# Performance work log

Hardware: AMD Instinct MI355X
Metric: run time of the kernel (lower is better)

## Reference

```python
import jax, jax.numpy as jnp
import numpy as np

NUM_NODES = 1_000_000
MEM_DIM = 128
MSG_DIM = 128
B = 262_144


def setup_inputs() -> dict:
    key = jax.random.key(0)
    k1, k2, k3, k4, k5, k6, k7 = jax.random.split(key, 7)
    s = 1.0 / np.sqrt(MEM_DIM)
    return {
        "memory": jax.random.normal(k1, (NUM_NODES, MEM_DIM), jnp.float32) * 0.1,
        "last_update": jnp.zeros((NUM_NODES,), jnp.float32),
        "messages": jax.random.normal(k2, (B, MSG_DIM), jnp.float32),
        "timestamps": jax.random.uniform(k3, (B,), jnp.float32),
        "W_ih": jax.random.uniform(k4, (3 * MEM_DIM, MSG_DIM), jnp.float32, -s, s),
        "W_hh": jax.random.uniform(k5, (3 * MEM_DIM, MEM_DIM), jnp.float32, -s, s),
        "b_ih": jax.random.uniform(k6, (3 * MEM_DIM,), jnp.float32, -s, s),
        "b_hh": jax.random.uniform(k7, (3 * MEM_DIM,), jnp.float32, -s, s),
        "node_ids": jax.random.randint(jax.random.fold_in(key, 99), (B,), 0, NUM_NODES, jnp.int64 if jax.config.jax_enable_x64 else jnp.int32),
    }


def gru_cell(x, h, W_ih, W_hh, b_ih, b_hh):
    # torch.nn.GRUCell math
    gi = x @ W_ih.T + b_ih  # [B, 3H]
    gh = h @ W_hh.T + b_hh  # [B, 3H]
    i_r, i_z, i_n = jnp.split(gi, 3, axis=-1)
    h_r, h_z, h_n = jnp.split(gh, 3, axis=-1)
    r = jax.nn.sigmoid(i_r + h_r)
    z = jax.nn.sigmoid(i_z + h_z)
    n = jnp.tanh(i_n + r * h_n)
    return (1.0 - z) * n + z * h


def reference(memory, last_update, messages, timestamps, W_ih, W_hh, b_ih, b_hh, node_ids):
    # gather node memory rows
    h = memory[node_ids]  # [B, MEM_DIM]
    h_new = gru_cell(messages, h, W_ih, W_hh, b_ih, b_hh)
    # scatter updated state and timestamps back into persistent buffers
    memory_new = memory.at[node_ids].set(h_new)
    last_update_new = last_update.at[node_ids].set(timestamps)
    return memory_new, last_update_new
```

## Files before the change

### kernel.cpp

```cpp
#include <hip/hip_runtime.h>
#include <hip/hip_bf16.h>
#include <stdint.h>

#define NN   1000000
#define DD   128
#define BT   262144
#define TR   64
#define RPB  512
#define NT   (RPB / TR)
#define GRUB (BT / RPB)
#define WINBIT (1 << 30)

typedef __attribute__((ext_vector_type(8))) short bf16x8;
typedef __attribute__((ext_vector_type(4))) float f32x4;

__device__ __forceinline__ uint32_t f2bf2(float lo, float hi) {
    __hip_bfloat162 b = __float22bfloat162_rn(make_float2(lo, hi));
    uint32_t u; __builtin_memcpy(&u, &b, 4); return u;
}
__device__ __forceinline__ bf16x8 cvt8(float4 a, float4 b) {
    union { bf16x8 v; uint32_t u[4]; } r;
    r.u[0] = f2bf2(a.x, a.y);
    r.u[1] = f2bf2(a.z, a.w);
    r.u[2] = f2bf2(b.x, b.y);
    r.u[3] = f2bf2(b.z, b.w);
    return r.v;
}
__device__ __forceinline__ float bf2f(unsigned short s) {
    union { uint32_t u; float f; } c; c.u = ((uint32_t)s) << 16;
    return c.f;
}
__device__ __forceinline__ float fastrcp(float x) {
    return __builtin_amdgcn_rcpf(x);
}
__device__ __forceinline__ float sigmoid_f(float x) {
    return fastrcp(1.0f + __expf(-x));
}
__device__ __forceinline__ float tanh_f(float x) {
    return fmaf(2.0f, fastrcp(1.0f + __expf(-2.0f * x)), -1.0f);
}

__global__ __launch_bounds__(256) void k_init(int4* __restrict__ winner) {
    int i = blockIdx.x * 256 + threadIdx.x;
    if (i < NN / 4) winner[i] = make_int4(-1, -1, -1, -1);
}

__global__ __launch_bounds__(256) void k_winner(const int* __restrict__ node_ids,
                                                int* __restrict__ winner) {
    int i = blockIdx.x * 256 + threadIdx.x;
    if (i < BT) atomicMax(&winner[node_ids[i]], i);
}

__global__ __launch_bounds__(256) void k_copy(const float4* __restrict__ mem_in,
                                              const float* __restrict__ lu_in,
                                              const float* __restrict__ ts,
                                              const int* __restrict__ winner,
                                              float4* __restrict__ mem_out,
                                              float* __restrict__ lu_out) {
    const long NV4 = (long)NN * 32;
    const long TOTAL = NV4 + NN;
    long stride = (long)gridDim.x * 256;
    for (long i = blockIdx.x * 256L + threadIdx.x; i < TOTAL; i += stride) {
        if (i < NV4) {
            int node = (int)(i >> 5);
            if (winner[node] < 0) mem_out[i] = mem_in[i];
        } else {
            int v = (int)(i - NV4);
            int w = winner[v];
            lu_out[v] = (w >= 0) ? ts[w] : lu_in[v];
        }
    }
}

__global__ __launch_bounds__(512, 2) void k_gru(const float* __restrict__ memory,
                                                const float* __restrict__ messages,
                                                const float* __restrict__ W_ih,
                                                const float* __restrict__ W_hh,
                                                const float* __restrict__ b_ih,
                                                const float* __restrict__ b_hh,
                                                const int* __restrict__ node_ids,
                                                const int* __restrict__ winner,
                                                float* __restrict__ out_mem) {
    __shared__ unsigned short x_lds[2][TR * DD];
    __shared__ unsigned short h_lds[2][TR * DD];
    __shared__ int s_nid[RPB];

    const int tid = threadIdx.x;
    const int rowBase = blockIdx.x * RPB;

    for (int i = tid; i < RPB; i += 512) {
        int brow = rowBase + i;
        int nid = node_ids[brow];
        s_nid[i] = nid | ((winner[nid] == brow) ? WINBIT : 0);
    }
    __syncthreads();

    const int lane  = tid & 63;
    const int wave  = tid >> 6;
    const int l15   = lane & 15;
    const int khalf = lane >> 4;
    const int jcol  = wave * 16 + l15;

    bf16x8 wf[6][4];
#pragma unroll
    for (int g = 0; g < 3; ++g) {
#pragma unroll
        for (int ks = 0; ks < 4; ++ks) {
            const float* p = W_ih + (size_t)(g * 128 + jcol) * DD + ks * 32 + khalf * 8;
            wf[g][ks] = cvt8(*(const float4*)p, *(const float4*)(p + 4));
            const float* q = W_hh + (size_t)(g * 128 + jcol) * DD + ks * 32 + khalf * 8;
            wf[3 + g][ks] = cvt8(*(const float4*)q, *(const float4*)(q + 4));
        }
    }
    const float br = b_ih[jcol] + b_hh[jcol];
    const float bz = b_ih[128 + jcol] + b_hh[128 + jcol];
    const float bin = b_ih[256 + jcol];
    const float bhn = b_hh[256 + jcol];

    const int sr  = tid >> 4;
    const int sc8 = (tid & 15) * 8;
    const int swz = (sc8 * 2) ^ ((sr & 7) << 4);
    const int offH0 = sr * 256 + swz;
    const int offH1 = (32 + sr) * 256 + swz;

#define GLOAD(X0, X1, H0, H1, t, half)                                          \
    {                                                                           \
        int r_ = (t) * TR + (half) * 32 + sr;                                   \
        const float* xp_ = messages + (size_t)(rowBase + r_) * DD + sc8;        \
        X0 = ((const float4*)xp_)[0]; X1 = ((const float4*)xp_)[1];             \
        const float* hp_ = memory + (size_t)(s_nid[r_] & (WINBIT - 1)) * DD + sc8; \
        H0 = ((const float4*)hp_)[0]; H1 = ((const float4*)hp_)[1];             \
    }

    float4 xA0, xA1, hA0, hA1, xB0, xB1, hB0, hB1;
    GLOAD(xA0, xA1, hA0, hA1, 0, 0);
    GLOAD(xB0, xB1, hB0, hB1, 0, 1);

#pragma unroll 1
    for (int t = 0; t < NT; ++t) {
        const int buf = t & 1;
        char* xb = (char*)(&x_lds[buf][0]);
        char* hb = (char*)(&h_lds[buf][0]);
        *(bf16x8*)(xb + offH0) = cvt8(xA0, xA1);
        *(bf16x8*)(hb + offH0) = cvt8(hA0, hA1);
        *(bf16x8*)(xb + offH1) = cvt8(xB0, xB1);
        *(bf16x8*)(hb + offH1) = cvt8(hB0, hB1);
        if (t + 1 < NT) {
            GLOAD(xA0, xA1, hA0, hA1, t + 1, 0);
            GLOAD(xB0, xB1, hB0, hB1, t + 1, 1);
        }
        asm volatile("s_waitcnt lgkmcnt(0)" ::: "memory");
        __builtin_amdgcn_sched_barrier(0);
        __builtin_amdgcn_s_barrier();
        __builtin_amdgcn_sched_barrier(0);

#pragma unroll
        for (int sub = 0; sub < 4; ++sub) {
            const int arow = sub * 16 + l15;
            const char* xr = (const char*)(&x_lds[buf][0]) + arow * 256;
            const char* hr = (const char*)(&h_lds[buf][0]) + arow * 256;
            const int aswz = (arow & 7) << 4;
            bf16x8 ax[4], ah[4];
#pragma unroll
            for (int ks = 0; ks < 4; ++ks) {
                const int cb = (ks * 64 + khalf * 16) ^ aswz;
                ax[ks] = *(const bf16x8*)(xr + cb);
                ah[ks] = *(const bf16x8*)(hr + cb);
            }
            f32x4 a_r  = {br,  br,  br,  br};
            f32x4 a_z  = {bz,  bz,  bz,  bz};
            f32x4 a_in = {bin, bin, bin, bin};
            f32x4 a_hn = {bhn, bhn, bhn, bhn};
#pragma unroll
            for (int ks = 0; ks < 4; ++ks) {
                a_r  = __builtin_amdgcn_mfma_f32_16x16x32_bf16(ax[ks], wf[0][ks], a_r,  0, 0, 0);
                a_r  = __builtin_amdgcn_mfma_f32_16x16x32_bf16(ah[ks], wf[3][ks], a_r,  0, 0, 0);
                a_z  = __builtin_amdgcn_mfma_f32_16x16x32_bf16(ax[ks], wf[1][ks], a_z,  0, 0, 0);
                a_z  = __builtin_amdgcn_mfma_f32_16x16x32_bf16(ah[ks], wf[4][ks], a_z,  0, 0, 0);
                a_in = __builtin_amdgcn_mfma_f32_16x16x32_bf16(ax[ks], wf[2][ks], a_in, 0, 0, 0);
                a_hn = __builtin_amdgcn_mfma_f32_16x16x32_bf16(ah[ks], wf[5][ks], a_hn, 0, 0, 0);
            }
#pragma unroll
            for (int q = 0; q < 4; ++q) {
                const int rl = sub * 16 + khalf * 4 + q;
                const int tr = t * TR + rl;
                float rg = sigmoid_f(a_r[q]);
                float zg = sigmoid_f(a_z[q]);
                float ng = tanh_f(a_in[q] + rg * a_hn[q]);
                unsigned short hu = *(const unsigned short*)(
                    (const char*)(&h_lds[buf][0]) + rl * 256 + ((jcol * 2) ^ ((rl & 7) << 4)));
                float h = bf2f(hu);
                float hnew = fmaf(zg, h - ng, ng);
                int v = s_nid[tr];
                if (v & WINBIT)
                    out_mem[(size_t)(v & (WINBIT - 1)) * DD + jcol] = hnew;
            }
        }
    }
#undef GLOAD
}

extern "C" void kernel_launch(void* const* d_in, const int* in_sizes, int n_in,
                              void* d_out, int out_size, void* d_ws, size_t ws_size,
                              hipStream_t stream) {
    const float* memory      = (const float*)d_in[0];
    const float* last_update = (const float*)d_in[1];
    const float* messages    = (const float*)d_in[2];
    const float* timestamps  = (const float*)d_in[3];
    const float* W_ih        = (const float*)d_in[4];
    const float* W_hh        = (const float*)d_in[5];
    const float* b_ih        = (const float*)d_in[6];
    const float* b_hh        = (const float*)d_in[7];
    const int*   node_ids    = (const int*)d_in[8];

    float* out_mem = (float*)d_out;
    float* out_lu  = out_mem + (size_t)NN * DD;

    int* winner = (int*)d_ws;

    k_init<<<(NN / 4 + 255) / 256, 256, 0, stream>>>((int4*)winner);
    k_winner<<<BT / 256, 256, 0, stream>>>(node_ids, winner);
    k_copy<<<4096, 256, 0, stream>>>((const float4*)memory, last_update, timestamps,
                                     winner, (float4*)out_mem, out_lu);
    k_gru<<<GRUB, 512, 0, stream>>>(memory, messages, W_ih, W_hh, b_ih, b_hh,
                                    node_ids, winner, out_mem);
}
```

Baseline: 282.9 us.

## Stage GRU inputs via direct global-to-LDS loads with fp32 tiles

Measured after the change: 493.0 us. 74.3% more time.

```diff
diff --git a/kernel.cpp b/kernel.cpp
--- a/kernel.cpp
+++ b/kernel.cpp
@@ -5,7 +5,7 @@
 #define NN   1000000
 #define DD   128
 #define BT   262144
-#define TR   64
+#define TR   32
 #define RPB  512
 #define NT   (RPB / TR)
 #define GRUB (BT / RPB)
@@ -26,9 +26,13 @@
     r.u[3] = f2bf2(b.z, b.w);
     return r.v;
 }
-__device__ __forceinline__ float bf2f(unsigned short s) {
-    union { uint32_t u; float f; } c; c.u = ((uint32_t)s) << 16;
-    return c.f;
+__device__ __forceinline__ bf16x8 cvt8v(f32x4 a, f32x4 b) {
+    union { bf16x8 v; uint32_t u[4]; } r;
+    r.u[0] = f2bf2(a[0], a[1]);
+    r.u[1] = f2bf2(a[2], a[3]);
+    r.u[2] = f2bf2(b[0], b[1]);
+    r.u[3] = f2bf2(b[2], b[3]);
+    return r.v;
 }
 __device__ __forceinline__ float fastrcp(float x) {
     return __builtin_amdgcn_rcpf(x);
@@ -38,6 +42,11 @@
 }
 __device__ __forceinline__ float tanh_f(float x) {
     return fmaf(2.0f, fastrcp(1.0f + __expf(-2.0f * x)), -1.0f);
+}
+__device__ __forceinline__ void glds16(const float* g, void* l) {
+    __builtin_amdgcn_global_load_lds(
+        (const __attribute__((address_space(1))) uint32_t*)g,
+        (__attribute__((address_space(3))) uint32_t*)l, 16, 0, 0);
 }
 
 __global__ __launch_bounds__(256) void k_init(int4* __restrict__ winner) {
@@ -72,7 +81,7 @@
     }
 }
 
-__global__ __launch_bounds__(512, 2) void k_gru(const float* __restrict__ memory,
+__global__ __launch_bounds__(512, 4) void k_gru(const float* __restrict__ memory,
                                                 const float* __restrict__ messages,
                                                 const float* __restrict__ W_ih,
                                                 const float* __restrict__ W_hh,
@@ -81,8 +90,8 @@
                                                 const int* __restrict__ node_ids,
                                                 const int* __restrict__ winner,
                                                 float* __restrict__ out_mem) {
-    __shared__ unsigned short x_lds[2][TR * DD];
-    __shared__ unsigned short h_lds[2][TR * DD];
+    __shared__ float x_lds[2][TR * DD];
+    __shared__ float h_lds[2][TR * DD];
     __shared__ int s_nid[RPB];
 
     const int tid = threadIdx.x;
@@ -112,73 +121,66 @@
             wf[3 + g][ks] = cvt8(*(const float4*)q, *(const float4*)(q + 4));
         }
     }
-    const float br = b_ih[jcol] + b_hh[jcol];
-    const float bz = b_ih[128 + jcol] + b_hh[128 + jcol];
+    const float br  = b_ih[jcol] + b_hh[jcol];
+    const float bz  = b_ih[128 + jcol] + b_hh[128 + jcol];
     const float bin = b_ih[256 + jcol];
     const float bhn = b_hh[256 + jcol];
 
-    const int sr  = tid >> 4;
-    const int sc8 = (tid & 15) * 8;
-    const int swz = (sc8 * 2) ^ ((sr & 7) << 4);
-    const int offH0 = sr * 256 + swz;
-    const int offH1 = (32 + sr) * 256 + swz;
-
-#define GLOAD(X0, X1, H0, H1, t, half)                                          \
-    {                                                                           \
-        int r_ = (t) * TR + (half) * 32 + sr;                                   \
-        const float* xp_ = messages + (size_t)(rowBase + r_) * DD + sc8;        \
-        X0 = ((const float4*)xp_)[0]; X1 = ((const float4*)xp_)[1];             \
-        const float* hp_ = memory + (size_t)(s_nid[r_] & (WINBIT - 1)) * DD + sc8; \
-        H0 = ((const float4*)hp_)[0]; H1 = ((const float4*)hp_)[1];             \
-    }
-
-    float4 xA0, xA1, hA0, hA1, xB0, xB1, hB0, hB1;
-    GLOAD(xA0, xA1, hA0, hA1, 0, 0);
-    GLOAD(xB0, xB1, hB0, hB1, 0, 1);
+    const int lrow0 = tid >> 5;
+    const int scc   = (tid & 31) ^ (lrow0 & 7);
+    const int ldsw0 = wave * 1024;
+    const int ldsw1 = wave * 1024 + 8192;
+
+#define STAGE(t, b)                                                              \
+    {                                                                            \
+        const int r0_ = (t) * TR + lrow0;                                        \
+        const float* xs0_ = messages + (size_t)(rowBase + r0_) * DD + scc * 4;   \
+        const float* xs1_ = messages + (size_t)(rowBase + r0_ + 16) * DD + scc * 4; \
+        const float* hs0_ = memory + (size_t)(s_nid[r0_] & (WINBIT - 1)) * DD + scc * 4; \
+        const float* hs1_ = memory + (size_t)(s_nid[r0_ + 16] & (WINBIT - 1)) * DD + scc * 4; \
+        glds16(xs0_, (char*)(&x_lds[b][0]) + ldsw0);                             \
+        glds16(xs1_, (char*)(&x_lds[b][0]) + ldsw1);                             \
+        glds16(hs0_, (char*)(&h_lds[b][0]) + ldsw0);                             \
+        glds16(hs1_, (char*)(&h_lds[b][0]) + ldsw1);                             \
+    }
+
+    STAGE(0, 0);
+    STAGE(1, 1);
 
 #pragma unroll 1
     for (int t = 0; t < NT; ++t) {
         const int buf = t & 1;
-        char* xb = (char*)(&x_lds[buf][0]);
-        char* hb = (char*)(&h_lds[buf][0]);
-        *(bf16x8*)(xb + offH0) = cvt8(xA0, xA1);
-        *(bf16x8*)(hb + offH0) = cvt8(hA0, hA1);
-        *(bf16x8*)(xb + offH1) = cvt8(xB0, xB1);
-        *(bf16x8*)(hb + offH1) = cvt8(hB0, hB1);
-        if (t + 1 < NT) {
-            GLOAD(xA0, xA1, hA0, hA1, t + 1, 0);
-            GLOAD(xB0, xB1, hB0, hB1, t + 1, 1);
-        }
-        asm volatile("s_waitcnt lgkmcnt(0)" ::: "memory");
+        if (t + 1 < NT) { asm volatile("s_waitcnt vmcnt(4)" ::: "memory"); }
+        else            { asm volatile("s_waitcnt vmcnt(0)" ::: "memory"); }
         __builtin_amdgcn_sched_barrier(0);
         __builtin_amdgcn_s_barrier();
         __builtin_amdgcn_sched_barrier(0);
 
 #pragma unroll
-        for (int sub = 0; sub < 4; ++sub) {
+        for (int sub = 0; sub < 2; ++sub) {
             const int arow = sub * 16 + l15;
-            const char* xr = (const char*)(&x_lds[buf][0]) + arow * 256;
-            const char* hr = (const char*)(&h_lds[buf][0]) + arow * 256;
-            const int aswz = (arow & 7) << 4;
-            bf16x8 ax[4], ah[4];
-#pragma unroll
-            for (int ks = 0; ks < 4; ++ks) {
-                const int cb = (ks * 64 + khalf * 16) ^ aswz;
-                ax[ks] = *(const bf16x8*)(xr + cb);
-                ah[ks] = *(const bf16x8*)(hr + cb);
-            }
+            const char* xb = (const char*)(&x_lds[buf][0]) + arow * 512;
+            const char* hb = (const char*)(&h_lds[buf][0]) + arow * 512;
+            const int as = arow & 7;
             f32x4 a_r  = {br,  br,  br,  br};
             f32x4 a_z  = {bz,  bz,  bz,  bz};
             f32x4 a_in = {bin, bin, bin, bin};
             f32x4 a_hn = {bhn, bhn, bhn, bhn};
 #pragma unroll
             for (int ks = 0; ks < 4; ++ks) {
-                a_r  = __builtin_amdgcn_mfma_f32_16x16x32_bf16(ax[ks], wf[0][ks], a_r,  0, 0, 0);
-                a_r  = __builtin_amdgcn_mfma_f32_16x16x32_bf16(ah[ks], wf[3][ks], a_r,  0, 0, 0);
-                a_z  = __builtin_amdgcn_mfma_f32_16x16x32_bf16(ax[ks], wf[1][ks], a_z,  0, 0, 0);
-                a_z  = __builtin_amdgcn_mfma_f32_16x16x32_bf16(ah[ks], wf[4][ks], a_z,  0, 0, 0);
-                a_in = __builtin_amdgcn_mfma_f32_16x16x32_bf16(ax[ks], wf[2][ks], a_in, 0, 0, 0);
-                a_hn = __builtin_amdgcn_mfma_f32_16x16x32_bf16(ah[ks], wf[5][ks], a_hn, 0, 0, 0);
+                const int c0 = ks * 8 + khalf * 2;
+                f32x4 x0 = *(const f32x4*)(xb + ((c0 ^ as) * 16));
+                f32x4 x1 = *(const f32x4*)(xb + (((c0 + 1) ^ as) * 16));
+                f32x4 h0 = *(const f32x4*)(hb + ((c0 ^ as) * 16));
+                f32x4 h1 = *(const f32x4*)(hb + (((c0 + 1) ^ as) * 16));
+                bf16x8 axk = cvt8v(x0, x1);
+                bf16x8 ahk = cvt8v(h0, h1);
+                a_r  = __builtin_amdgcn_mfma_f32_16x16x32_bf16(axk, wf[0][ks], a_r,  0, 0, 0);
+                a_r  = __builtin_amdgcn_mfma_f32_16x16x32_bf16(ahk, wf[3][ks], a_r,  0, 0, 0);
+                a_z  = __builtin_amdgcn_mfma_f32_16x16x32_bf16(axk, wf[1][ks], a_z,  0, 0, 0);
+                a_z  = __builtin_amdgcn_mfma_f32_16x16x32_bf16(ahk, wf[4][ks], a_z,  0, 0, 0);
+                a_in = __builtin_amdgcn_mfma_f32_16x16x32_bf16(axk, wf[2][ks], a_in, 0, 0, 0);
+                a_hn = __builtin_amdgcn_mfma_f32_16x16x32_bf16(ahk, wf[5][ks], a_hn, 0, 0, 0);
             }
 #pragma unroll
             for (int q = 0; q < 4; ++q) {
@@ -187,17 +189,20 @@
                 float rg = sigmoid_f(a_r[q]);
                 float zg = sigmoid_f(a_z[q]);
                 float ng = tanh_f(a_in[q] + rg * a_hn[q]);
-                unsigned short hu = *(const unsigned short*)(
-                    (const char*)(&h_lds[buf][0]) + rl * 256 + ((jcol * 2) ^ ((rl & 7) << 4)));
-                float h = bf2f(hu);
+                float h = h_lds[buf][rl * 128 + (((jcol >> 2) ^ (rl & 7)) * 4) + (jcol & 3)];
                 float hnew = fmaf(zg, h - ng, ng);
                 int v = s_nid[tr];
                 if (v & WINBIT)
                     out_mem[(size_t)(v & (WINBIT - 1)) * DD + jcol] = hnew;
             }
         }
-    }
-#undef GLOAD
+
+        __builtin_amdgcn_sched_barrier(0);
+        __builtin_amdgcn_s_barrier();
+        __builtin_amdgcn_sched_barrier(0);
+        if (t + 2 < NT) STAGE(t + 2, buf);
+    }
+#undef STAGE
 }
 
 extern "C" void kernel_launch(void* const* d_in, const int* in_sizes, int n_in,
```

## Fuse bulk memory copy and last_update scatter into GRU kernel

Applied to the files above, without the earlier changes.

After: 462.2 us. 63.4% more time.

```diff
diff --git a/kernel.cpp b/kernel.cpp
--- a/kernel.cpp
+++ b/kernel.cpp
@@ -10,6 +10,7 @@
 #define NT   (RPB / TR)
 #define GRUB (BT / RPB)
 #define WINBIT (1 << 30)
+#define NV4  32000000L
 
 typedef __attribute__((ext_vector_type(8))) short bf16x8;
 typedef __attribute__((ext_vector_type(4))) float f32x4;
@@ -49,27 +50,6 @@
                                                 int* __restrict__ winner) {
     int i = blockIdx.x * 256 + threadIdx.x;
     if (i < BT) atomicMax(&winner[node_ids[i]], i);
-}
-
-__global__ __launch_bounds__(256) void k_copy(const float4* __restrict__ mem_in,
-                                              const float* __restrict__ lu_in,
-                                              const float* __restrict__ ts,
-                                              const int* __restrict__ winner,
-                                              float4* __restrict__ mem_out,
-                                              float* __restrict__ lu_out) {
-    const long NV4 = (long)NN * 32;
-    const long TOTAL = NV4 + NN;
-    long stride = (long)gridDim.x * 256;
-    for (long i = blockIdx.x * 256L + threadIdx.x; i < TOTAL; i += stride) {
-        if (i < NV4) {
-            int node = (int)(i >> 5);
-            if (winner[node] < 0) mem_out[i] = mem_in[i];
-        } else {
-            int v = (int)(i - NV4);
-            int w = winner[v];
-            lu_out[v] = (w >= 0) ? ts[w] : lu_in[v];
-        }
-    }
 }
 
 __global__ __launch_bounds__(512, 2) void k_gru(const float* __restrict__ memory,
@@ -80,7 +60,10 @@
                                                 const float* __restrict__ b_hh,
                                                 const int* __restrict__ node_ids,
                                                 const int* __restrict__ winner,
-                                                float* __restrict__ out_mem) {
+                                                const float* __restrict__ lu_in,
+                                                const float* __restrict__ ts,
+                                                float* __restrict__ out_mem,
+                                                float* __restrict__ out_lu) {
     __shared__ unsigned short x_lds[2][TR * DD];
     __shared__ unsigned short h_lds[2][TR * DD];
     __shared__ int s_nid[RPB];
@@ -112,8 +95,8 @@
             wf[3 + g][ks] = cvt8(*(const float4*)q, *(const float4*)(q + 4));
         }
     }
-    const float br = b_ih[jcol] + b_hh[jcol];
-    const float bz = b_ih[128 + jcol] + b_hh[128 + jcol];
+    const float br  = b_ih[jcol] + b_hh[jcol];
+    const float bz  = b_ih[128 + jcol] + b_hh[128 + jcol];
     const float bin = b_ih[256 + jcol];
     const float bhn = b_hh[256 + jcol];
 
@@ -122,6 +105,9 @@
     const int swz = (sc8 * 2) ^ ((sr & 7) << 4);
     const int offH0 = sr * 256 + swz;
     const int offH1 = (32 + sr) * 256 + swz;
+
+    const float4* mem4 = (const float4*)memory;
+    float4* out4 = (float4*)out_mem;
 
 #define GLOAD(X0, X1, H0, H1, t, half)                                          \
     {                                                                           \
@@ -196,8 +182,22 @@
                     out_mem[(size_t)(v & (WINBIT - 1)) * DD + jcol] = hnew;
             }
         }
+
+        {
+            const long base4 = ((long)(blockIdx.x * NT + t)) * 8192 + tid;
+#pragma unroll
+            for (int k = 0; k < 16; ++k) {
+                long f = base4 + (long)k * 512;
+                if (f < NV4 && winner[(int)(f >> 5)] < 0) out4[f] = mem4[f];
+            }
+        }
     }
 #undef GLOAD
+
+    for (int i = blockIdx.x * 512 + tid; i < NN; i += GRUB * 512) {
+        int w = winner[i];
+        out_lu[i] = (w >= 0) ? ts[w] : lu_in[i];
+    }
 }
 
 extern "C" void kernel_launch(void* const* d_in, const int* in_sizes, int n_in,
@@ -220,8 +220,7 @@
 
     k_init<<<(NN / 4 + 255) / 256, 256, 0, stream>>>((int4*)winner);
     k_winner<<<BT / 256, 256, 0, stream>>>(node_ids, winner);
-    k_copy<<<4096, 256, 0, stream>>>((const float4*)memory, last_update, timestamps,
-                                     winner, (float4*)out_mem, out_lu);
     k_gru<<<GRUB, 512, 0, stream>>>(memory, messages, W_ih, W_hh, b_ih, b_hh,
-                                    node_ids, winner, out_mem);
-}
+                                    node_ids, winner, last_update, timestamps,
+                                    out_mem, out_lu);
+}
```

## Reorder gather prefetch in GRU loop, ping-pong h registers, raise occupancy bound

Applied to the files above, without the earlier changes.

Measured after the change: 508.6 us. +79.8%, slower.

```diff
diff --git a/kernel.cpp b/kernel.cpp
--- a/kernel.cpp
+++ b/kernel.cpp
@@ -72,7 +72,7 @@
     }
 }
 
-__global__ __launch_bounds__(512, 2) void k_gru(const float* __restrict__ memory,
+__global__ __launch_bounds__(512, 4) void k_gru(const float* __restrict__ memory,
                                                 const float* __restrict__ messages,
                                                 const float* __restrict__ W_ih,
                                                 const float* __restrict__ W_hh,
@@ -112,8 +112,8 @@
             wf[3 + g][ks] = cvt8(*(const float4*)q, *(const float4*)(q + 4));
         }
     }
-    const float br = b_ih[jcol] + b_hh[jcol];
-    const float bz = b_ih[128 + jcol] + b_hh[128 + jcol];
+    const float br  = b_ih[jcol] + b_hh[jcol];
+    const float bz  = b_ih[128 + jcol] + b_hh[128 + jcol];
     const float bin = b_ih[256 + jcol];
     const float bhn = b_hh[256 + jcol];
 
@@ -123,81 +123,101 @@
     const int offH0 = sr * 256 + swz;
     const int offH1 = (32 + sr) * 256 + swz;
 
-#define GLOAD(X0, X1, H0, H1, t, half)                                          \
+#define GLOADX(t)                                                               \
     {                                                                           \
-        int r_ = (t) * TR + (half) * 32 + sr;                                   \
-        const float* xp_ = messages + (size_t)(rowBase + r_) * DD + sc8;        \
-        X0 = ((const float4*)xp_)[0]; X1 = ((const float4*)xp_)[1];             \
-        const float* hp_ = memory + (size_t)(s_nid[r_] & (WINBIT - 1)) * DD + sc8; \
-        H0 = ((const float4*)hp_)[0]; H1 = ((const float4*)hp_)[1];             \
-    }
-
-    float4 xA0, xA1, hA0, hA1, xB0, xB1, hB0, hB1;
-    GLOAD(xA0, xA1, hA0, hA1, 0, 0);
-    GLOAD(xB0, xB1, hB0, hB1, 0, 1);
+        int r_ = (t) * TR + sr;                                                 \
+        const float* xp0_ = messages + (size_t)(rowBase + r_) * DD + sc8;       \
+        const float* xp1_ = messages + (size_t)(rowBase + r_ + 32) * DD + sc8;  \
+        xA0 = ((const float4*)xp0_)[0]; xA1 = ((const float4*)xp0_)[1];         \
+        xB0 = ((const float4*)xp1_)[0]; xB1 = ((const float4*)xp1_)[1];         \
+    }
+#define GLOADH(H0, H1, H2, H3, t)                                               \
+    {                                                                           \
+        int r_ = (t) * TR + sr;                                                 \
+        const float* hp0_ = memory + (size_t)(s_nid[r_] & (WINBIT - 1)) * DD + sc8; \
+        const float* hp1_ = memory + (size_t)(s_nid[r_ + 32] & (WINBIT - 1)) * DD + sc8; \
+        H0 = ((const float4*)hp0_)[0]; H1 = ((const float4*)hp0_)[1];           \
+        H2 = ((const float4*)hp1_)[0]; H3 = ((const float4*)hp1_)[1];           \
+    }
+
+    float4 xA0, xA1, xB0, xB1;
+    float4 hP0, hP1, hP2, hP3, hQ0, hQ1, hQ2, hQ3;
+
+    GLOADH(hP0, hP1, hP2, hP3, 0);
+    GLOADX(0);
+
+#define BODY(t, HC0, HC1, HC2, HC3, HN0, HN1, HN2, HN3)                         \
+    {                                                                           \
+        const int buf = (t) & 1;                                                \
+        char* xb = (char*)(&x_lds[buf][0]);                                     \
+        char* hb = (char*)(&h_lds[buf][0]);                                     \
+                        \
+        if ((t) + 1 < NT) GLOADH(HN0, HN1, HN2, HN3, (t) + 1);                  \
+             \
+        *(bf16x8*)(xb + offH0) = cvt8(xA0, xA1);                                \
+        *(bf16x8*)(xb + offH1) = cvt8(xB0, xB1);                                \
+        if ((t) + 1 < NT) GLOADX((t) + 1);                                      \
+                                            \
+        *(bf16x8*)(hb + offH0) = cvt8(HC0, HC1);                                \
+        *(bf16x8*)(hb + offH1) = cvt8(HC2, HC3);                                \
+                          \
+        asm volatile("s_waitcnt lgkmcnt(0)" ::: "memory");                      \
+        __builtin_amdgcn_sched_barrier(0);                                      \
+        __builtin_amdgcn_s_barrier();                                           \
+        __builtin_amdgcn_sched_barrier(0);                                      \
+                                          \
+        _Pragma("unroll")                                                       \
+        for (int sub = 0; sub < 4; ++sub) {                                     \
+            const int arow = sub * 16 + l15;                                    \
+            const char* xr = (const char*)(&x_lds[buf][0]) + arow * 256;        \
+            const char* hr = (const char*)(&h_lds[buf][0]) + arow * 256;        \
+            const int aswz = (arow & 7) << 4;                                   \
+            bf16x8 ax[4], ah[4];                                                \
+            _Pragma("unroll")                                                   \
+            for (int ks = 0; ks < 4; ++ks) {                                    \
+                const int cb = (ks * 64 + khalf * 16) ^ aswz;                   \
+                ax[ks] = *(const bf16x8*)(xr + cb);                             \
+                ah[ks] = *(const bf16x8*)(hr + cb);                             \
+            }                                                                   \
+            f32x4 a_r  = {br,  br,  br,  br};                                   \
+            f32x4 a_z  = {bz,  bz,  bz,  bz};                                   \
+            f32x4 a_in = {bin, bin, bin, bin};                                  \
+            f32x4 a_hn = {bhn, bhn, bhn, bhn};                                  \
+            _Pragma("unroll")                                                   \
+            for (int ks = 0; ks < 4; ++ks) {                                    \
+                a_r  = __builtin_amdgcn_mfma_f32_16x16x32_bf16(ax[ks], wf[0][ks], a_r,  0, 0, 0); \
+                a_r  = __builtin_amdgcn_mfma_f32_16x16x32_bf16(ah[ks], wf[3][ks], a_r,  0, 0, 0); \
+                a_z  = __builtin_amdgcn_mfma_f32_16x16x32_bf16(ax[ks], wf[1][ks], a_z,  0, 0, 0); \
+                a_z  = __builtin_amdgcn_mfma_f32_16x16x32_bf16(ah[ks], wf[4][ks], a_z,  0, 0, 0); \
+                a_in = __builtin_amdgcn_mfma_f32_16x16x32_bf16(ax[ks], wf[2][ks], a_in, 0, 0, 0); \
+                a_hn = __builtin_amdgcn_mfma_f32_16x16x32_bf16(ah[ks], wf[5][ks], a_hn, 0, 0, 0); \
+            }                                                                   \
+            _Pragma("unroll")                                                   \
+            for (int q = 0; q < 4; ++q) {                                       \
+                const int rl = sub * 16 + khalf * 4 + q;                        \
+                const int tr = (t) * TR + rl;                                   \
+                float rg = sigmoid_f(a_r[q]);                                   \
+                float zg = sigmoid_f(a_z[q]);                                   \
+                float ng = tanh_f(a_in[q] + rg * a_hn[q]);                      \
+                unsigned short hu = *(const unsigned short*)(                   \
+                    (const char*)(&h_lds[buf][0]) + rl * 256 + ((jcol * 2) ^ ((rl & 7) << 4))); \
+                float h = bf2f(hu);                                             \
+                float hnew = fmaf(zg, h - ng, ng);                              \
+                int v = s_nid[tr];                                              \
+                if (v & WINBIT)                                                 \
+                    out_mem[(size_t)(v & (WINBIT - 1)) * DD + jcol] = hnew;     \
+            }                                                                   \
+        }                                                                       \
+    }
 
 #pragma unroll 1
-    for (int t = 0; t < NT; ++t) {
-        const int buf = t & 1;
-        char* xb = (char*)(&x_lds[buf][0]);
-        char* hb = (char*)(&h_lds[buf][0]);
-        *(bf16x8*)(xb + offH0) = cvt8(xA0, xA1);
-        *(bf16x8*)(hb + offH0) = cvt8(hA0, hA1);
-        *(bf16x8*)(xb + offH1) = cvt8(xB0, xB1);
-        *(bf16x8*)(hb + offH1) = cvt8(hB0, hB1);
-        if (t + 1 < NT) {
-            GLOAD(xA0, xA1, hA0, hA1, t + 1, 0);
-            GLOAD(xB0, xB1, hB0, hB1, t + 1, 1);
-        }
-        asm volatile("s_waitcnt lgkmcnt(0)" ::: "memory");
-        __builtin_amdgcn_sched_barrier(0);
-        __builtin_amdgcn_s_barrier();
-        __builtin_amdgcn_sched_barrier(0);
-
-#pragma unroll
-        for (int sub = 0; sub < 4; ++sub) {
-            const int arow = sub * 16 + l15;
-            const char* xr = (const char*)(&x_lds[buf][0]) + arow * 256;
-            const char* hr = (const char*)(&h_lds[buf][0]) + arow * 256;
-            const int aswz = (arow & 7) << 4;
-            bf16x8 ax[4], ah[4];
-#pragma unroll
-            for (int ks = 0; ks < 4; ++ks) {
-                const int cb = (ks * 64 + khalf * 16) ^ aswz;
-                ax[ks] = *(const bf16x8*)(xr + cb);
-                ah[ks] = *(const bf16x8*)(hr + cb);
-            }
-            f32x4 a_r  = {br,  br,  br,  br};
-            f32x4 a_z  = {bz,  bz,  bz,  bz};
-            f32x4 a_in = {bin, bin, bin, bin};
-            f32x4 a_hn = {bhn, bhn, bhn, bhn};
-#pragma unroll
-            for (int ks = 0; ks < 4; ++ks) {
-                a_r  = __builtin_amdgcn_mfma_f32_16x16x32_bf16(ax[ks], wf[0][ks], a_r,  0, 0, 0);
-                a_r  = __builtin_amdgcn_mfma_f32_16x16x32_bf16(ah[ks], wf[3][ks], a_r,  0, 0, 0);
-                a_z  = __builtin_amdgcn_mfma_f32_16x16x32_bf16(ax[ks], wf[1][ks], a_z,  0, 0, 0);
-                a_z  = __builtin_amdgcn_mfma_f32_16x16x32_bf16(ah[ks], wf[4][ks], a_z,  0, 0, 0);
-                a_in = __builtin_amdgcn_mfma_f32_16x16x32_bf16(ax[ks], wf[2][ks], a_in, 0, 0, 0);
-                a_hn = __builtin_amdgcn_mfma_f32_16x16x32_bf16(ah[ks], wf[5][ks], a_hn, 0, 0, 0);
-            }
-#pragma unroll
-            for (int q = 0; q < 4; ++q) {
-                const int rl = sub * 16 + khalf * 4 + q;
-                const int tr = t * TR + rl;
-                float rg = sigmoid_f(a_r[q]);
-                float zg = sigmoid_f(a_z[q]);
-                float ng = tanh_f(a_in[q] + rg * a_hn[q]);
-                unsigned short hu = *(const unsigned short*)(
-                    (const char*)(&h_lds[buf][0]) + rl * 256 + ((jcol * 2) ^ ((rl & 7) << 4)));
-                float h = bf2f(hu);
-                float hnew = fmaf(zg, h - ng, ng);
-                int v = s_nid[tr];
-                if (v & WINBIT)
-                    out_mem[(size_t)(v & (WINBIT - 1)) * DD + jcol] = hnew;
-            }
-        }
-    }
-#undef GLOAD
+    for (int tp = 0; tp < NT; tp += 2) {
+        BODY(tp,     hP0, hP1, hP2, hP3, hQ0, hQ1, hQ2, hQ3);
+        BODY(tp + 1, hQ0, hQ1, hQ2, hQ3, hP0, hP1, hP2, hP3);
+    }
+#undef BODY
+#undef GLOADX
+#undef GLOADH
 }
 
 extern "C" void kernel_launch(void* const* d_in, const int* in_sizes, int n_in,
```
